# Optimization experiments

Measured on AMD Instinct MI355X. Metric: run time of the kernel, lower is better.

The kernel has to match this reference:

```python
import jax, jax.numpy as jnp
import numpy as np

B, C, D, H, W = 2, 64, 8, 24, 24  # hidden_dim = C; N = D*H*W = 4608 tokens


def setup_inputs() -> dict:
    key = jax.random.key(0)
    ks = jax.random.split(key, 8)
    s = 1.0 / np.sqrt(C)  # fan-in style init for 1x1 conv weights
    return {
        "x": jax.random.normal(ks[0], (B, C, D, H, W), dtype=jnp.float32),
        "h": jax.random.normal(ks[1], (B, C, D, H, W), dtype=jnp.float32),
        "Wq": jax.random.normal(ks[2], (C, C), dtype=jnp.float32) * s,
        "bq": jax.random.normal(ks[3], (C,), dtype=jnp.float32) * s,
        "Wk": jax.random.normal(ks[4], (C, C), dtype=jnp.float32) * s,
        "bk": jax.random.normal(ks[5], (C,), dtype=jnp.float32) * s,
        "Wv": jax.random.normal(ks[6], (C, C), dtype=jnp.float32) * s,
        "bv": jax.random.normal(ks[7], (C,), dtype=jnp.float32) * s,
    }


def reference(x, h, Wq, bq, Wk, bk, Wv, bv):
    # 1x1 Conv3d == per-token linear over channels
    def proj(inp, Wt, bt):
        f = inp.reshape(inp.shape[0], inp.shape[1], -1)  # [B, C, N]
        return jnp.einsum('oc,bcn->bon', Wt, f) + bt[None, :, None]

    q = proj(x, Wq, bq)  # [B, C, N]
    k = proj(h, Wk, bk)  # [B, C, N]
    v = proj(h, Wv, bv)  # [B, C, N]

    scale = 1.0 / np.sqrt(k.shape[1])  # k.size(1) ** 0.5 == sqrt(C)
    scores = jnp.einsum('bcm,bcn->bmn', q, k) * scale  # [B, N, N]
    attn = jax.nn.softmax(scores, axis=-1)
    out = jnp.einsum('bcn,bmn->bcm', v, attn)  # [B, C, N]
    return out.reshape(h.shape)
```

## Files before the change

### kernel.cpp

```cpp
#include <hip/hip_runtime.h>
#include <hip/hip_bf16.h>

#define C_DIM 64
#define N_TOK 4608
#define NBLK  72
#define B_SZ  2
#define M64BLKS 72
#define NSEG  8
#define SEGLEN (N_TOK / NSEG)
#define KTILES 288
#define VTILES 72
#define OSTR  68

typedef __bf16 bf16x8 __attribute__((ext_vector_type(8)));
typedef float  f32x4  __attribute__((ext_vector_type(4)));


__device__ __forceinline__ void gemm_tile(
    const __hip_bfloat16* wmat, const bf16x8 bin[2], const float* bias,
    int col, int quad, f32x4 acc[4])
{
    #pragma unroll
    for (int ot = 0; ot < 4; ot++) {
        f32x4 a = (f32x4){0.f, 0.f, 0.f, 0.f};
        #pragma unroll
        for (int kh = 0; kh < 2; kh++) {
            bf16x8 wf = *(const bf16x8*)(wmat + (ot * 16 + col) * 72 +
                                         kh * 32 + quad * 8);
            a = __builtin_amdgcn_mfma_f32_16x16x32_bf16(wf, bin[kh], a, 0, 0, 0);
        }
        float4 b4 = *(const float4*)(bias + ot * 16 + quad * 4);
        a[0] += b4.x; a[1] += b4.y; a[2] += b4.z; a[3] += b4.w;
        acc[ot] = a;
    }
}

__global__ __launch_bounds__(256) void proj_kernel(
    const float* __restrict__ x,  const float* __restrict__ h,
    const float* __restrict__ Wq, const float* __restrict__ bq,
    const float* __restrict__ Wk, const float* __restrict__ bk,
    const float* __restrict__ Wv, const float* __restrict__ bv,
    __hip_bfloat16* __restrict__ qS, __hip_bfloat16* __restrict__ kS,
    __hip_bfloat16* __restrict__ vS)
{
    __shared__ __hip_bfloat16 wl[3 * 64 * 72];
    __shared__ __hip_bfloat16 xt[64 * 72];
    __shared__ __hip_bfloat16 ht[64 * 72];
    __shared__ __hip_bfloat16 vl[64 * 72];

    const int b  = blockIdx.x / NBLK;
    const int n0 = (blockIdx.x % NBLK) * 64;
    const int t  = threadIdx.x;

    #pragma unroll
    for (int mat = 0; mat < 3; mat++) {
        const float* W = (mat == 0) ? Wq : ((mat == 1) ? Wk : Wv);
        __hip_bfloat16* wd = wl + mat * (64 * 72);
        #pragma unroll
        for (int i = 0; i < 4; i++) {
            const int ch = i * 256 + t;
            const int o = ch >> 4, c0 = (ch & 15) * 4;
            float4 w4 = *(const float4*)(W + ch * 4);
            union { __hip_bfloat16 e[4]; uint2 v; } pk;
            pk.e[0] = __float2bfloat16(w4.x); pk.e[1] = __float2bfloat16(w4.y);
            pk.e[2] = __float2bfloat16(w4.z); pk.e[3] = __float2bfloat16(w4.w);
            *(uint2*)(wd + o * 72 + c0) = pk.v;
        }
    }
    #pragma unroll
    for (int i = 0; i < 4; i++) {
        const int ch = i * 256 + t;
        const int c = ch >> 4, n4 = (ch & 15) * 4;
        float4 x4 = *(const float4*)(x + (size_t)(b * C_DIM + c) * N_TOK + n0 + n4);
        float4 h4 = *(const float4*)(h + (size_t)(b * C_DIM + c) * N_TOK + n0 + n4);
        xt[(n4 + 0) * 72 + c] = __float2bfloat16(x4.x);
        xt[(n4 + 1) * 72 + c] = __float2bfloat16(x4.y);
        xt[(n4 + 2) * 72 + c] = __float2bfloat16(x4.z);
        xt[(n4 + 3) * 72 + c] = __float2bfloat16(x4.w);
        ht[(n4 + 0) * 72 + c] = __float2bfloat16(h4.x);
        ht[(n4 + 1) * 72 + c] = __float2bfloat16(h4.y);
        ht[(n4 + 2) * 72 + c] = __float2bfloat16(h4.z);
        ht[(n4 + 3) * 72 + c] = __float2bfloat16(h4.w);
    }
    __syncthreads();

    const int wave = t >> 6, lane = t & 63;
    const int col = lane & 15, quad = lane >> 4;

    bf16x8 xb[2], hb[2];
    #pragma unroll
    for (int kh = 0; kh < 2; kh++) {
        xb[kh] = *(const bf16x8*)(xt + (wave * 16 + col) * 72 + kh * 32 + quad * 8);
        hb[kh] = *(const bf16x8*)(ht + (wave * 16 + col) * 72 + kh * 32 + quad * 8);
    }

    f32x4 acc[4];

    gemm_tile(wl + 0 * (64 * 72), xb, bq, col, quad, acc);
    {
        const size_t tile16 = (size_t)b * KTILES + (n0 >> 4) + wave;
        const float SC = 0.125f * 1.44269504088896f;
        #pragma unroll
        for (int ot = 0; ot < 4; ot++) {
            union { __hip_bfloat16 e[4]; uint2 v; } pk;
            #pragma unroll
            for (int r = 0; r < 4; r++) pk.e[r] = __float2bfloat16(acc[ot][r] * SC);
            *(uint2*)(qS + (tile16 << 10) + (ot >> 1) * 512 +
                      ((ot * 2 + (quad >> 1)) & 3) * 128 + col * 8 +
                      (quad & 1) * 4) = pk.v;
        }
    }

    gemm_tile(wl + 1 * (64 * 72), hb, bk, col, quad, acc);
    {
        const int t_l = (wave >> 1) * 2 + ((col >> 2) & 1);
        const int row = ((wave * 2 + (col >> 3)) & 3) * 4 + (col & 3);
        const size_t tile16 = (size_t)b * KTILES + (n0 >> 4) + t_l;
        #pragma unroll
        for (int ot = 0; ot < 4; ot++) {
            union { __hip_bfloat16 e[4]; uint2 v; } pk;
            #pragma unroll
            for (int r = 0; r < 4; r++) pk.e[r] = __float2bfloat16(acc[ot][r]);
            *(uint2*)(kS + (tile16 << 10) + (ot >> 1) * 512 +
                      ((ot * 2 + (quad >> 1)) & 3) * 128 + row * 8 +
                      (quad & 1) * 4) = pk.v;
        }
    }

    gemm_tile(wl + 2 * (64 * 72), hb, bv, col, quad, acc);
    #pragma unroll
    for (int ot = 0; ot < 4; ot++)
        #pragma unroll
        for (int r = 0; r < 4; r++)
            vl[(ot * 16 + quad * 4 + r) * 72 + wave * 16 + col] =
                __float2bfloat16(acc[ot][r]);
    __syncthreads();
    {
        const size_t vbase = ((size_t)(b * VTILES) + (n0 >> 6)) << 12;
        #pragma unroll
        for (int rep = 0; rep < 2; rep++) {
            const int ch = rep * 256 + t;
            const int cc = ch >> 7, hf = (ch >> 6) & 1;
            const int qd = (ch >> 4) & 3, c2 = ch & 15;
            *(uint4*)(vS + vbase + (size_t)ch * 8) =
                *(const uint4*)(vl + (cc * 16 + c2) * 72 + hf * 32 + qd * 8);
        }
    }
}

__global__ __launch_bounds__(512) void attn_kernel(
    const __hip_bfloat16* __restrict__ qS,
    const __hip_bfloat16* __restrict__ kS,
    const __hip_bfloat16* __restrict__ vS,
    float* __restrict__ out)
{
    __shared__ float o_lds[NSEG * 16 * OSTR];
    __shared__ float lstat[NSEG][64];

    const int b    = blockIdx.x / M64BLKS;
    const int mblk = blockIdx.x % M64BLKS;
    const int wave = threadIdx.x >> 6;
    const int lane = threadIdx.x & 63;
    const int col  = lane & 15;
    const int quad = lane >> 4;
    const int m0   = mblk * 64;

    const __hip_bfloat16* qp =
        qS + (((size_t)b * KTILES + (m0 >> 4)) << 10) + lane * 8;
    bf16x8 qa[4][2];
    #pragma unroll
    for (int ms = 0; ms < 4; ms++) {
        qa[ms][0] = *(const bf16x8*)(qp + ms * 1024);
        qa[ms][1] = *(const bf16x8*)(qp + ms * 1024 + 512);
    }

    f32x4 accO[4][4];
    #pragma unroll
    for (int ms = 0; ms < 4; ms++)
        #pragma unroll
        for (int cc = 0; cc < 4; cc++)
            accO[ms][cc] = (f32x4){0.f, 0.f, 0.f, 0.f};
    float rsum[4] = {0.f, 0.f, 0.f, 0.f};

    const int nbeg = wave * SEGLEN;

    #pragma unroll 1
    for (int n0 = nbeg; n0 < nbeg + SEGLEN; n0 += 64) {
        const __hip_bfloat16* kt =
            kS + (((size_t)b * KTILES + (n0 >> 4)) << 10) + lane * 8;
        bf16x8 ka[8];
        #pragma unroll
        for (int j = 0; j < 4; j++) {
            ka[2 * j]     = *(const bf16x8*)(kt + (j << 10));
            ka[2 * j + 1] = *(const bf16x8*)(kt + (j << 10) + 512);
        }
        const __hip_bfloat16* vt =
            vS + ((((size_t)b * VTILES) + (n0 >> 6)) << 12) + lane * 8;
        bf16x8 va[8];
        #pragma unroll
        for (int cc = 0; cc < 4; cc++) {
            va[2 * cc]     = *(const bf16x8*)(vt + cc * 1024);
            va[2 * cc + 1] = *(const bf16x8*)(vt + cc * 1024 + 512);
        }

        #pragma unroll
        for (int ms = 0; ms < 4; ms++) {
            f32x4 s[4];
            #pragma unroll
            for (int j = 0; j < 4; j++) {
                s[j] = __builtin_amdgcn_mfma_f32_16x16x32_bf16(
                           ka[2 * j], qa[ms][0], (f32x4){0.f, 0.f, 0.f, 0.f}, 0, 0, 0);
                s[j] = __builtin_amdgcn_mfma_f32_16x16x32_bf16(
                           ka[2 * j + 1], qa[ms][1], s[j], 0, 0, 0);
            }
            union { __hip_bfloat16 e[8]; bf16x8 v; } p0, p1;
            float ps = 0.f;
            #pragma unroll
            for (int j = 0; j < 2; j++)
                #pragma unroll
                for (int r = 0; r < 4; r++) {
                    float e0 = __builtin_amdgcn_exp2f(s[j][r]);
                    float e1 = __builtin_amdgcn_exp2f(s[2 + j][r]);
                    ps += e0 + e1;
                    p0.e[j * 4 + r] = __float2bfloat16(e0);
                    p1.e[j * 4 + r] = __float2bfloat16(e1);
                }
            rsum[ms] += ps;
            #pragma unroll
            for (int cc = 0; cc < 4; cc++) {
                accO[ms][cc] = __builtin_amdgcn_mfma_f32_16x16x32_bf16(
                                   va[2 * cc], p0.v, accO[ms][cc], 0, 0, 0);
                accO[ms][cc] = __builtin_amdgcn_mfma_f32_16x16x32_bf16(
                                   va[2 * cc + 1], p1.v, accO[ms][cc], 0, 0, 0);
            }
        }
    }

    #pragma unroll
    for (int ms = 0; ms < 4; ms++) {
        rsum[ms] += __shfl_xor(rsum[ms], 16);
        rsum[ms] += __shfl_xor(rsum[ms], 32);
    }
    if (quad == 0) {
        #pragma unroll
        for (int ms = 0; ms < 4; ms++) lstat[wave][ms * 16 + col] = rsum[ms];
    }

    #pragma unroll
    for (int phase = 0; phase < 4; phase++) {
        #pragma unroll
        for (int cc = 0; cc < 4; cc++)
            *(f32x4*)(o_lds + (wave * 16 + col) * OSTR + cc * 16 + quad * 4) =
                accO[phase][cc];
        __syncthreads();
        if (threadIdx.x < 256) {
            const int m  = threadIdx.x & 15;
            const int cq = threadIdx.x >> 4;
            const int mi = phase * 16 + m;
            float lsum = 0.f;
            f32x4 oacc = (f32x4){0.f, 0.f, 0.f, 0.f};
            #pragma unroll
            for (int sgm = 0; sgm < NSEG; sgm++) {
                lsum += lstat[sgm][mi];
                oacc += *(const f32x4*)(o_lds + (sgm * 16 + m) * OSTR + cq * 4);
            }
            const float inv = 1.0f / lsum;
            #pragma unroll
            for (int r = 0; r < 4; r++) {
                const int c = cq * 4 + r;
                out[(size_t)(b * C_DIM + c) * N_TOK + m0 + phase * 16 + m] =
                    oacc[r] * inv;
            }
        }
        __syncthreads();
    }
}

extern "C" void kernel_launch(void* const* d_in, const int* in_sizes, int n_in,
                              void* d_out, int out_size, void* d_ws, size_t ws_size,
                              hipStream_t stream) {
    const float* x  = (const float*)d_in[0];
    const float* h  = (const float*)d_in[1];
    const float* Wq = (const float*)d_in[2];
    const float* bq = (const float*)d_in[3];
    const float* Wk = (const float*)d_in[4];
    const float* bk = (const float*)d_in[5];
    const float* Wv = (const float*)d_in[6];
    const float* bv = (const float*)d_in[7];
    float* out = (float*)d_out;

    const size_t elems = (size_t)B_SZ * N_TOK * C_DIM;
    __hip_bfloat16* qS = (__hip_bfloat16*)d_ws;
    __hip_bfloat16* kS = qS + elems;
    __hip_bfloat16* vS = kS + elems;

    proj_kernel<<<B_SZ * NBLK, 256, 0, stream>>>(x, h, Wq, bq, Wk, bk, Wv, bv,
                                                 qS, kS, vS);
    attn_kernel<<<B_SZ * M64BLKS, 512, 0, stream>>>(qS, kS, vS, out);
}
```

Baseline: 93.16 us.

## Double-buffer K/V tiles into LDS via async global_load_lds with 32-token steps

Replaces the per-iteration direct global loads of K and V fragments into registers with asynchronous global-to-LDS copies into a per-wave double buffer, prefetching the next 32-token tile while computing the current one. The inner step shrinks from 64 to 32 tokens, which cuts the fragment registers needed and packs P into a single bf16x8 per m-subtile. The goal is to hide global memory latency and lower register pressure. In exchange it uses 128KB of LDS per block, which may limit occupancy to one block per CU, and adds a barrier before the reduction so the staging buffers can be reused as o_lds.

```diff
diff --git a/kernel.cpp b/kernel.cpp
--- a/kernel.cpp
+++ b/kernel.cpp
@@ -8,6 +8,7 @@
 #define M64BLKS 72
 #define NSEG  8
 #define SEGLEN (N_TOK / NSEG)
+#define NT32  (SEGLEN / 32)
 #define KTILES 288
 #define VTILES 72
 #define OSTR  68
@@ -15,6 +16,12 @@
 typedef __bf16 bf16x8 __attribute__((ext_vector_type(8)));
 typedef float  f32x4  __attribute__((ext_vector_type(4)));
 
+
+__device__ __forceinline__ void gll16(const void* g, void* l) {
+    __builtin_amdgcn_global_load_lds(
+        (const __attribute__((address_space(1))) void*)g,
+        (__attribute__((address_space(3))) void*)l, 16, 0, 0);
+}
 
 __device__ __forceinline__ void gemm_tile(
     const __hip_bfloat16* wmat, const bf16x8 bin[2], const float* bias,
@@ -154,8 +161,9 @@
     const __hip_bfloat16* __restrict__ vS,
     float* __restrict__ out)
 {
-    __shared__ float o_lds[NSEG * 16 * OSTR];
-    __shared__ float lstat[NSEG][64];
+    __shared__ __align__(16) char smem[NSEG * 16384];
+    float* o_lds = (float*)smem;
+    float* lstat = (float*)(smem + NSEG * 16 * OSTR * 4);
 
     const int b    = blockIdx.x / M64BLKS;
     const int mblk = blockIdx.x % M64BLKS;
@@ -183,56 +191,74 @@
     float rsum[4] = {0.f, 0.f, 0.f, 0.f};
 
     const int nbeg = wave * SEGLEN;
+    char* sbase = smem + wave * 16384;
+    const __hip_bfloat16* kbb = kS + (((size_t)b * KTILES) << 10) + lane * 8;
+    const __hip_bfloat16* vbb = vS + (((size_t)b * VTILES) << 12) + lane * 8;
+
+    auto stage = [&](int t, int p) {
+        const int n0 = nbeg + t * 32;
+        char* dst = sbase + p * 8192;
+        const __hip_bfloat16* kt = kbb + ((size_t)(n0 >> 4) << 10);
+        #pragma unroll
+        for (int j = 0; j < 2; j++) {
+            gll16(kt + (j << 10),       dst + j * 2048);
+            gll16(kt + (j << 10) + 512, dst + j * 2048 + 1024);
+        }
+        const __hip_bfloat16* vt = vbb + ((size_t)(n0 >> 6) << 12) +
+                                   ((n0 >> 5) & 1) * 512;
+        #pragma unroll
+        for (int cc = 0; cc < 4; cc++)
+            gll16(vt + cc * 1024, dst + 4096 + cc * 1024);
+    };
+
+    stage(0, 0);
 
     #pragma unroll 1
-    for (int n0 = nbeg; n0 < nbeg + SEGLEN; n0 += 64) {
-        const __hip_bfloat16* kt =
-            kS + (((size_t)b * KTILES + (n0 >> 4)) << 10) + lane * 8;
-        bf16x8 ka[8];
-        #pragma unroll
-        for (int j = 0; j < 4; j++) {
-            ka[2 * j]     = *(const bf16x8*)(kt + (j << 10));
-            ka[2 * j + 1] = *(const bf16x8*)(kt + (j << 10) + 512);
-        }
-        const __hip_bfloat16* vt =
-            vS + ((((size_t)b * VTILES) + (n0 >> 6)) << 12) + lane * 8;
-        bf16x8 va[8];
-        #pragma unroll
-        for (int cc = 0; cc < 4; cc++) {
-            va[2 * cc]     = *(const bf16x8*)(vt + cc * 1024);
-            va[2 * cc + 1] = *(const bf16x8*)(vt + cc * 1024 + 512);
-        }
+    for (int t = 0; t < NT32; t++) {
+        const int p = t & 1;
+        if (t + 1 < NT32) {
+            stage(t + 1, p ^ 1);
+            asm volatile("s_waitcnt vmcnt(8)" ::: "memory");
+        } else {
+            asm volatile("s_waitcnt vmcnt(0)" ::: "memory");
+        }
+        __builtin_amdgcn_sched_barrier(0);
+
+        const char* buf = sbase + p * 8192;
+        bf16x8 ka[4], va[4];
+        #pragma unroll
+        for (int j = 0; j < 2; j++) {
+            ka[2 * j]     = *(const bf16x8*)(buf + j * 2048 + lane * 16);
+            ka[2 * j + 1] = *(const bf16x8*)(buf + j * 2048 + 1024 + lane * 16);
+        }
+        #pragma unroll
+        for (int cc = 0; cc < 4; cc++)
+            va[cc] = *(const bf16x8*)(buf + 4096 + cc * 1024 + lane * 16);
 
         #pragma unroll
         for (int ms = 0; ms < 4; ms++) {
-            f32x4 s[4];
-            #pragma unroll
-            for (int j = 0; j < 4; j++) {
-                s[j] = __builtin_amdgcn_mfma_f32_16x16x32_bf16(
-                           ka[2 * j], qa[ms][0], (f32x4){0.f, 0.f, 0.f, 0.f}, 0, 0, 0);
-                s[j] = __builtin_amdgcn_mfma_f32_16x16x32_bf16(
-                           ka[2 * j + 1], qa[ms][1], s[j], 0, 0, 0);
+            f32x4 s0 = __builtin_amdgcn_mfma_f32_16x16x32_bf16(
+                           ka[0], qa[ms][0], (f32x4){0.f, 0.f, 0.f, 0.f}, 0, 0, 0);
+            s0 = __builtin_amdgcn_mfma_f32_16x16x32_bf16(ka[1], qa[ms][1], s0, 0, 0, 0);
+            f32x4 s1 = __builtin_amdgcn_mfma_f32_16x16x32_bf16(
+                           ka[2], qa[ms][0], (f32x4){0.f, 0.f, 0.f, 0.f}, 0, 0, 0);
+            s1 = __builtin_amdgcn_mfma_f32_16x16x32_bf16(ka[3], qa[ms][1], s1, 0, 0, 0);
+
+            union { __hip_bfloat16 e[8]; bf16x8 v; } pk;
+            float ps = 0.f;
+            #pragma unroll
+            for (int r = 0; r < 4; r++) {
+                float e0 = __builtin_amdgcn_exp2f(s0[r]);
+                float e1 = __builtin_amdgcn_exp2f(s1[r]);
+                ps += e0 + e1;
+                pk.e[r]     = __float2bfloat16(e0);
+                pk.e[4 + r] = __float2bfloat16(e1);
             }
-            union { __hip_bfloat16 e[8]; bf16x8 v; } p0, p1;
-            float ps = 0.f;
-            #pragma unroll
-            for (int j = 0; j < 2; j++)
-                #pragma unroll
-                for (int r = 0; r < 4; r++) {
-                    float e0 = __builtin_amdgcn_exp2f(s[j][r]);
-                    float e1 = __builtin_amdgcn_exp2f(s[2 + j][r]);
-                    ps += e0 + e1;
-                    p0.e[j * 4 + r] = __float2bfloat16(e0);
-                    p1.e[j * 4 + r] = __float2bfloat16(e1);
-                }
             rsum[ms] += ps;
             #pragma unroll
-            for (int cc = 0; cc < 4; cc++) {
+            for (int cc = 0; cc < 4; cc++)
                 accO[ms][cc] = __builtin_amdgcn_mfma_f32_16x16x32_bf16(
-                                   va[2 * cc], p0.v, accO[ms][cc], 0, 0, 0);
-                accO[ms][cc] = __builtin_amdgcn_mfma_f32_16x16x32_bf16(
-                                   va[2 * cc + 1], p1.v, accO[ms][cc], 0, 0, 0);
-            }
+                                   va[cc], pk.v, accO[ms][cc], 0, 0, 0);
         }
     }
 
@@ -241,9 +267,12 @@
         rsum[ms] += __shfl_xor(rsum[ms], 16);
         rsum[ms] += __shfl_xor(rsum[ms], 32);
     }
+
+    __syncthreads();
+
     if (quad == 0) {
         #pragma unroll
-        for (int ms = 0; ms < 4; ms++) lstat[wave][ms * 16 + col] = rsum[ms];
+        for (int ms = 0; ms < 4; ms++) lstat[wave * 64 + ms * 16 + col] = rsum[ms];
     }
 
     #pragma unroll
@@ -261,7 +290,7 @@
             f32x4 oacc = (f32x4){0.f, 0.f, 0.f, 0.f};
             #pragma unroll
             for (int sgm = 0; sgm < NSEG; sgm++) {
-                lsum += lstat[sgm][mi];
+                lsum += lstat[sgm * 64 + mi];
                 oacc += *(const f32x4*)(o_lds + (sgm * 16 + m) * OSTR + cq * 4);
             }
             const float inv = 1.0f / lsum;
```

Result: slower. 95.78 us (+2.8%).

## Split attention key range across blocks and add normalization reduction kernel

Applied to the files above, without the earlier changes.

Each attention block now covers 128 query rows, with two wave groups of 64, and one third of the key range, so the grid grows from 144 to 216 blocks. Partial unnormalized outputs and row sums go to workspace buffers. A new norm_kernel sums the three partials and divides by the row sum. This aims to fill more compute units and shorten the serial key loop per wave, at the cost of extra global traffic for the partials and one more kernel launch.

```diff
diff --git a/kernel.cpp b/kernel.cpp
--- a/kernel.cpp
+++ b/kernel.cpp
@@ -5,9 +5,11 @@
 #define N_TOK 4608
 #define NBLK  72
 #define B_SZ  2
-#define M64BLKS 72
-#define NSEG  8
-#define SEGLEN (N_TOK / NSEG)
+#define M128BLKS 36
+#define NSPLIT 3
+#define NSEG  4
+#define SEGLEN 384
+#define NT    6
 #define KTILES 288
 #define VTILES 72
 #define OSTR  68
@@ -152,18 +154,26 @@
     const __hip_bfloat16* __restrict__ qS,
     const __hip_bfloat16* __restrict__ kS,
     const __hip_bfloat16* __restrict__ vS,
-    float* __restrict__ out)
+    float* __restrict__ Pb, float* __restrict__ Lb)
 {
-    __shared__ float o_lds[NSEG * 16 * OSTR];
-    __shared__ float lstat[NSEG][64];
-
-    const int b    = blockIdx.x / M64BLKS;
-    const int mblk = blockIdx.x % M64BLKS;
+    __shared__ float o_lds[2][NSEG][16][OSTR];
+    __shared__ float lstat[2][NSEG][64];
+
+    const int idx  = blockIdx.x;
+    const int b    = idx / (M128BLKS * NSPLIT);
+    const int rem  = idx % (M128BLKS * NSPLIT);
+    const int mblk = rem / NSPLIT;
+    const int ns   = rem % NSPLIT;
     const int wave = threadIdx.x >> 6;
     const int lane = threadIdx.x & 63;
     const int col  = lane & 15;
     const int quad = lane >> 4;
-    const int m0   = mblk * 64;
+    const int mg   = wave >> 2;
+    const int seg  = wave & 3;
+    const int m0   = mblk * 128 + mg * 64;
+
+    float* Pns = Pb + (size_t)ns * (B_SZ * C_DIM * N_TOK);
+    float* Lns = Lb + (size_t)ns * (B_SZ * N_TOK);
 
     const __hip_bfloat16* qp =
         qS + (((size_t)b * KTILES + (m0 >> 4)) << 10) + lane * 8;
@@ -182,10 +192,11 @@
             accO[ms][cc] = (f32x4){0.f, 0.f, 0.f, 0.f};
     float rsum[4] = {0.f, 0.f, 0.f, 0.f};
 
-    const int nbeg = wave * SEGLEN;
+    const int nbeg = ns * (NSEG * SEGLEN) + seg * SEGLEN;
 
     #pragma unroll 1
-    for (int n0 = nbeg; n0 < nbeg + SEGLEN; n0 += 64) {
+    for (int t = 0; t < NT; t++) {
+        const int n0 = nbeg + t * 64;
         const __hip_bfloat16* kt =
             kS + (((size_t)b * KTILES + (n0 >> 4)) << 10) + lane * 8;
         bf16x8 ka[8];
@@ -209,7 +220,8 @@
             #pragma unroll
             for (int j = 0; j < 4; j++) {
                 s[j] = __builtin_amdgcn_mfma_f32_16x16x32_bf16(
-                           ka[2 * j], qa[ms][0], (f32x4){0.f, 0.f, 0.f, 0.f}, 0, 0, 0);
+                           ka[2 * j], qa[ms][0],
+                           (f32x4){0.f, 0.f, 0.f, 0.f}, 0, 0, 0);
                 s[j] = __builtin_amdgcn_mfma_f32_16x16x32_bf16(
                            ka[2 * j + 1], qa[ms][1], s[j], 0, 0, 0);
             }
@@ -243,37 +255,58 @@
     }
     if (quad == 0) {
         #pragma unroll
-        for (int ms = 0; ms < 4; ms++) lstat[wave][ms * 16 + col] = rsum[ms];
-    }
-
-    #pragma unroll
-    for (int phase = 0; phase < 4; phase++) {
+        for (int ms = 0; ms < 4; ms++) lstat[mg][seg][ms * 16 + col] = rsum[ms];
+    }
+
+    #pragma unroll
+    for (int p = 0; p < 4; p++) {
         #pragma unroll
         for (int cc = 0; cc < 4; cc++)
-            *(f32x4*)(o_lds + (wave * 16 + col) * OSTR + cc * 16 + quad * 4) =
-                accO[phase][cc];
+            *(f32x4*)(&o_lds[mg][seg][col][cc * 16 + quad * 4]) = accO[p][cc];
         __syncthreads();
-        if (threadIdx.x < 256) {
-            const int m  = threadIdx.x & 15;
-            const int cq = threadIdx.x >> 4;
-            const int mi = phase * 16 + m;
-            float lsum = 0.f;
-            f32x4 oacc = (f32x4){0.f, 0.f, 0.f, 0.f};
-            #pragma unroll
-            for (int sgm = 0; sgm < NSEG; sgm++) {
-                lsum += lstat[sgm][mi];
-                oacc += *(const f32x4*)(o_lds + (sgm * 16 + m) * OSTR + cq * 4);
-            }
-            const float inv = 1.0f / lsum;
-            #pragma unroll
-            for (int r = 0; r < 4; r++) {
-                const int c = cq * 4 + r;
-                out[(size_t)(b * C_DIM + c) * N_TOK + m0 + phase * 16 + m] =
-                    oacc[r] * inv;
-            }
+        {
+            const int t   = threadIdx.x;
+            const int mgR = t >> 8;
+            const int c   = (t >> 2) & 63;
+            const int mq  = t & 3;
+            f32x4 os = (f32x4){0.f, 0.f, 0.f, 0.f};
+            f32x4 ls = (f32x4){0.f, 0.f, 0.f, 0.f};
+            #pragma unroll
+            for (int sgm = 0; sgm < NSEG; sgm++)
+                #pragma unroll
+                for (int j = 0; j < 4; j++) {
+                    os[j] += o_lds[mgR][sgm][mq * 4 + j][c];
+                    ls[j] += lstat[mgR][sgm][p * 16 + mq * 4 + j];
+                }
+            const int mabs = mblk * 128 + mgR * 64 + p * 16 + mq * 4;
+            *(f32x4*)(Pns + ((size_t)b * C_DIM + c) * N_TOK + mabs) = os;
+            if (c == 0)
+                *(f32x4*)(Lns + (size_t)b * N_TOK + mabs) = ls;
         }
         __syncthreads();
     }
+}
+
+__global__ __launch_bounds__(256) void norm_kernel(
+    const float* __restrict__ Pb, const float* __restrict__ Lb,
+    float* __restrict__ out)
+{
+    const size_t stride = (size_t)B_SZ * C_DIM * N_TOK;
+    const size_t f = ((size_t)blockIdx.x * 256 + threadIdx.x) * 4;
+    f32x4 o = *(const f32x4*)(Pb + f) +
+              *(const f32x4*)(Pb + stride + f) +
+              *(const f32x4*)(Pb + 2 * stride + f);
+    const int b = (int)(f / ((size_t)C_DIM * N_TOK));
+    const int m = (int)(f % N_TOK);
+    const size_t lf = (size_t)b * N_TOK + m;
+    const size_t lstride = (size_t)B_SZ * N_TOK;
+    f32x4 l = *(const f32x4*)(Lb + lf) +
+              *(const f32x4*)(Lb + lstride + lf) +
+              *(const f32x4*)(Lb + 2 * lstride + lf);
+    f32x4 r;
+    #pragma unroll
+    for (int j = 0; j < 4; j++) r[j] = o[j] / l[j];
+    *(f32x4*)(out + f) = r;
 }
 
 extern "C" void kernel_launch(void* const* d_in, const int* in_sizes, int n_in,
@@ -293,8 +326,11 @@
     __hip_bfloat16* qS = (__hip_bfloat16*)d_ws;
     __hip_bfloat16* kS = qS + elems;
     __hip_bfloat16* vS = kS + elems;
+    float* Pb = (float*)(vS + elems);
+    float* Lb = Pb + NSPLIT * elems;
 
     proj_kernel<<<B_SZ * NBLK, 256, 0, stream>>>(x, h, Wq, bq, Wk, bk, Wv, bv,
                                                  qS, kS, vS);
-    attn_kernel<<<B_SZ * M64BLKS, 512, 0, stream>>>(qS, kS, vS, out);
-}
+    attn_kernel<<<B_SZ * M128BLKS * NSPLIT, 512, 0, stream>>>(qS, kS, vS, Pb, Lb);
+    norm_kernel<<<576, 256, 0, stream>>>(Pb, Lb, out);
+}
```

Result: no change. 92.31 us (median of 2 runs) (-0.9%).

## Fuse projection and attention into one cooperative kernel with grid sync

Applied to the files above, without the earlier changes.

Merges the projection and attention kernels into a single cooperative launch of 144 blocks of 512 threads. A grid-wide barrier separates writing Q/K/V to workspace from the attention phase. The projection is split so four waves compute Q while the other four compute K and V, and shared memory is aliased between the two phases. This removes the second kernel launch and the gap between kernels, at the cost of a grid sync and cooperative-launch overhead.

```diff
diff --git a/kernel.cpp b/kernel.cpp
--- a/kernel.cpp
+++ b/kernel.cpp
@@ -1,13 +1,14 @@
 #include <hip/hip_runtime.h>
+#include <hip/hip_cooperative_groups.h>
 #include <hip/hip_bf16.h>
 
 #define C_DIM 64
 #define N_TOK 4608
 #define NBLK  72
 #define B_SZ  2
-#define M64BLKS 72
 #define NSEG  8
 #define SEGLEN (N_TOK / NSEG)
+#define NT64  (SEGLEN / 64)
 #define KTILES 288
 #define VTILES 72
 #define OSTR  68
@@ -15,6 +16,8 @@
 typedef __bf16 bf16x8 __attribute__((ext_vector_type(8)));
 typedef float  f32x4  __attribute__((ext_vector_type(4)));
 
+
+namespace cg = cooperative_groups;
 
 __device__ __forceinline__ void gemm_tile(
     const __hip_bfloat16* wmat, const bf16x8 bin[2], const float* bias,
@@ -35,30 +38,34 @@
     }
 }
 
-__global__ __launch_bounds__(256) void proj_kernel(
+__global__ __launch_bounds__(512) void fused_kernel(
     const float* __restrict__ x,  const float* __restrict__ h,
     const float* __restrict__ Wq, const float* __restrict__ bq,
     const float* __restrict__ Wk, const float* __restrict__ bk,
     const float* __restrict__ Wv, const float* __restrict__ bv,
     __hip_bfloat16* __restrict__ qS, __hip_bfloat16* __restrict__ kS,
-    __hip_bfloat16* __restrict__ vS)
+    __hip_bfloat16* __restrict__ vS, float* __restrict__ out)
 {
-    __shared__ __hip_bfloat16 wl[3 * 64 * 72];
-    __shared__ __hip_bfloat16 xt[64 * 72];
-    __shared__ __hip_bfloat16 ht[64 * 72];
-    __shared__ __hip_bfloat16 vl[64 * 72];
-
-    const int b  = blockIdx.x / NBLK;
-    const int n0 = (blockIdx.x % NBLK) * 64;
-    const int t  = threadIdx.x;
+    __shared__ __align__(16) char smraw[55296];
+    __hip_bfloat16* wl = (__hip_bfloat16*)smraw;
+    __hip_bfloat16* xt = (__hip_bfloat16*)(smraw + 27648);
+    __hip_bfloat16* ht = (__hip_bfloat16*)(smraw + 36864);
+    __hip_bfloat16* vl = (__hip_bfloat16*)(smraw + 46080);
+    float* o_lds = (float*)smraw;
+    float* lstat = (float*)(smraw + 34816);
+
+    const int b   = blockIdx.x / NBLK;
+    const int nb  = blockIdx.x % NBLK;
+    const int t   = threadIdx.x;
+    const int n0b = nb * 64;
 
     #pragma unroll
     for (int mat = 0; mat < 3; mat++) {
         const float* W = (mat == 0) ? Wq : ((mat == 1) ? Wk : Wv);
         __hip_bfloat16* wd = wl + mat * (64 * 72);
         #pragma unroll
-        for (int i = 0; i < 4; i++) {
-            const int ch = i * 256 + t;
+        for (int i = 0; i < 2; i++) {
+            const int ch = i * 512 + t;
             const int o = ch >> 4, c0 = (ch & 15) * 4;
             float4 w4 = *(const float4*)(W + ch * 4);
             union { __hip_bfloat16 e[4]; uint2 v; } pk;
@@ -68,11 +75,11 @@
         }
     }
     #pragma unroll
-    for (int i = 0; i < 4; i++) {
-        const int ch = i * 256 + t;
+    for (int i = 0; i < 2; i++) {
+        const int ch = i * 512 + t;
         const int c = ch >> 4, n4 = (ch & 15) * 4;
-        float4 x4 = *(const float4*)(x + (size_t)(b * C_DIM + c) * N_TOK + n0 + n4);
-        float4 h4 = *(const float4*)(h + (size_t)(b * C_DIM + c) * N_TOK + n0 + n4);
+        float4 x4 = *(const float4*)(x + (size_t)(b * C_DIM + c) * N_TOK + n0b + n4);
+        float4 h4 = *(const float4*)(h + (size_t)(b * C_DIM + c) * N_TOK + n0b + n4);
         xt[(n4 + 0) * 72 + c] = __float2bfloat16(x4.x);
         xt[(n4 + 1) * 72 + c] = __float2bfloat16(x4.y);
         xt[(n4 + 2) * 72 + c] = __float2bfloat16(x4.z);
@@ -87,18 +94,15 @@
     const int wave = t >> 6, lane = t & 63;
     const int col = lane & 15, quad = lane >> 4;
 
-    bf16x8 xb[2], hb[2];
-    #pragma unroll
-    for (int kh = 0; kh < 2; kh++) {
-        xb[kh] = *(const bf16x8*)(xt + (wave * 16 + col) * 72 + kh * 32 + quad * 8);
-        hb[kh] = *(const bf16x8*)(ht + (wave * 16 + col) * 72 + kh * 32 + quad * 8);
-    }
-
-    f32x4 acc[4];
-
-    gemm_tile(wl + 0 * (64 * 72), xb, bq, col, quad, acc);
-    {
-        const size_t tile16 = (size_t)b * KTILES + (n0 >> 4) + wave;
+    if (wave < 4) {
+        bf16x8 xb[2];
+        #pragma unroll
+        for (int kh = 0; kh < 2; kh++)
+            xb[kh] = *(const bf16x8*)(xt + (wave * 16 + col) * 72 +
+                                      kh * 32 + quad * 8);
+        f32x4 acc[4];
+        gemm_tile(wl, xb, bq, col, quad, acc);
+        const size_t tile16 = (size_t)b * KTILES + (n0b >> 4) + wave;
         const float SC = 0.125f * 1.44269504088896f;
         #pragma unroll
         for (int ot = 0; ot < 4; ot++) {
@@ -109,61 +113,50 @@
                       ((ot * 2 + (quad >> 1)) & 3) * 128 + col * 8 +
                       (quad & 1) * 4) = pk.v;
         }
-    }
-
-    gemm_tile(wl + 1 * (64 * 72), hb, bk, col, quad, acc);
-    {
-        const int t_l = (wave >> 1) * 2 + ((col >> 2) & 1);
-        const int row = ((wave * 2 + (col >> 3)) & 3) * 4 + (col & 3);
-        const size_t tile16 = (size_t)b * KTILES + (n0 >> 4) + t_l;
-        #pragma unroll
-        for (int ot = 0; ot < 4; ot++) {
-            union { __hip_bfloat16 e[4]; uint2 v; } pk;
-            #pragma unroll
-            for (int r = 0; r < 4; r++) pk.e[r] = __float2bfloat16(acc[ot][r]);
-            *(uint2*)(kS + (tile16 << 10) + (ot >> 1) * 512 +
-                      ((ot * 2 + (quad >> 1)) & 3) * 128 + row * 8 +
-                      (quad & 1) * 4) = pk.v;
-        }
-    }
-
-    gemm_tile(wl + 2 * (64 * 72), hb, bv, col, quad, acc);
-    #pragma unroll
-    for (int ot = 0; ot < 4; ot++)
-        #pragma unroll
-        for (int r = 0; r < 4; r++)
-            vl[(ot * 16 + quad * 4 + r) * 72 + wave * 16 + col] =
-                __float2bfloat16(acc[ot][r]);
+    } else {
+        const int wv = wave - 4;
+        bf16x8 hb[2];
+        #pragma unroll
+        for (int kh = 0; kh < 2; kh++)
+            hb[kh] = *(const bf16x8*)(ht + (wv * 16 + col) * 72 +
+                                      kh * 32 + quad * 8);
+        f32x4 acc[4];
+        gemm_tile(wl + 1 * (64 * 72), hb, bk, col, quad, acc);
+        {
+            const int t_l = (wv >> 1) * 2 + ((col >> 2) & 1);
+            const int row = ((wv * 2 + (col >> 3)) & 3) * 4 + (col & 3);
+            const size_t tile16 = (size_t)b * KTILES + (n0b >> 4) + t_l;
+            #pragma unroll
+            for (int ot = 0; ot < 4; ot++) {
+                union { __hip_bfloat16 e[4]; uint2 v; } pk;
+                #pragma unroll
+                for (int r = 0; r < 4; r++) pk.e[r] = __float2bfloat16(acc[ot][r]);
+                *(uint2*)(kS + (tile16 << 10) + (ot >> 1) * 512 +
+                          ((ot * 2 + (quad >> 1)) & 3) * 128 + row * 8 +
+                          (quad & 1) * 4) = pk.v;
+            }
+        }
+        gemm_tile(wl + 2 * (64 * 72), hb, bv, col, quad, acc);
+        #pragma unroll
+        for (int ot = 0; ot < 4; ot++)
+            #pragma unroll
+            for (int r = 0; r < 4; r++)
+                vl[(ot * 16 + quad * 4 + r) * 72 + wv * 16 + col] =
+                    __float2bfloat16(acc[ot][r]);
+    }
     __syncthreads();
     {
-        const size_t vbase = ((size_t)(b * VTILES) + (n0 >> 6)) << 12;
-        #pragma unroll
-        for (int rep = 0; rep < 2; rep++) {
-            const int ch = rep * 256 + t;
-            const int cc = ch >> 7, hf = (ch >> 6) & 1;
-            const int qd = (ch >> 4) & 3, c2 = ch & 15;
-            *(uint4*)(vS + vbase + (size_t)ch * 8) =
-                *(const uint4*)(vl + (cc * 16 + c2) * 72 + hf * 32 + qd * 8);
-        }
-    }
-}
-
-__global__ __launch_bounds__(512) void attn_kernel(
-    const __hip_bfloat16* __restrict__ qS,
-    const __hip_bfloat16* __restrict__ kS,
-    const __hip_bfloat16* __restrict__ vS,
-    float* __restrict__ out)
-{
-    __shared__ float o_lds[NSEG * 16 * OSTR];
-    __shared__ float lstat[NSEG][64];
-
-    const int b    = blockIdx.x / M64BLKS;
-    const int mblk = blockIdx.x % M64BLKS;
-    const int wave = threadIdx.x >> 6;
-    const int lane = threadIdx.x & 63;
-    const int col  = lane & 15;
-    const int quad = lane >> 4;
-    const int m0   = mblk * 64;
+        const size_t vbase = ((size_t)(b * VTILES) + (n0b >> 6)) << 12;
+        const int cc = t >> 7, hf = (t >> 6) & 1;
+        const int qd = (t >> 4) & 3, c2 = t & 15;
+        *(uint4*)(vS + vbase + (size_t)t * 8) =
+            *(const uint4*)(vl + (cc * 16 + c2) * 72 + hf * 32 + qd * 8);
+    }
+
+    __threadfence();
+    cg::this_grid().sync();
+
+    const int m0 = nb * 64;
 
     const __hip_bfloat16* qp =
         qS + (((size_t)b * KTILES + (m0 >> 4)) << 10) + lane * 8;
@@ -185,7 +178,8 @@
     const int nbeg = wave * SEGLEN;
 
     #pragma unroll 1
-    for (int n0 = nbeg; n0 < nbeg + SEGLEN; n0 += 64) {
+    for (int tt = 0; tt < NT64; tt++) {
+        const int n0 = nbeg + tt * 64;
         const __hip_bfloat16* kt =
             kS + (((size_t)b * KTILES + (n0 >> 4)) << 10) + lane * 8;
         bf16x8 ka[8];
@@ -209,7 +203,8 @@
             #pragma unroll
             for (int j = 0; j < 4; j++) {
                 s[j] = __builtin_amdgcn_mfma_f32_16x16x32_bf16(
-                           ka[2 * j], qa[ms][0], (f32x4){0.f, 0.f, 0.f, 0.f}, 0, 0, 0);
+                           ka[2 * j], qa[ms][0],
+                           (f32x4){0.f, 0.f, 0.f, 0.f}, 0, 0, 0);
                 s[j] = __builtin_amdgcn_mfma_f32_16x16x32_bf16(
                            ka[2 * j + 1], qa[ms][1], s[j], 0, 0, 0);
             }
@@ -241,9 +236,10 @@
         rsum[ms] += __shfl_xor(rsum[ms], 16);
         rsum[ms] += __shfl_xor(rsum[ms], 32);
     }
+    __syncthreads();
     if (quad == 0) {
         #pragma unroll
-        for (int ms = 0; ms < 4; ms++) lstat[wave][ms * 16 + col] = rsum[ms];
+        for (int ms = 0; ms < 4; ms++) lstat[wave * 64 + ms * 16 + col] = rsum[ms];
     }
 
     #pragma unroll
@@ -261,7 +257,7 @@
             f32x4 oacc = (f32x4){0.f, 0.f, 0.f, 0.f};
             #pragma unroll
             for (int sgm = 0; sgm < NSEG; sgm++) {
-                lsum += lstat[sgm][mi];
+                lsum += lstat[sgm * 64 + mi];
                 oacc += *(const f32x4*)(o_lds + (sgm * 16 + m) * OSTR + cq * 4);
             }
             const float inv = 1.0f / lsum;
@@ -294,7 +290,9 @@
     __hip_bfloat16* kS = qS + elems;
     __hip_bfloat16* vS = kS + elems;
 
-    proj_kernel<<<B_SZ * NBLK, 256, 0, stream>>>(x, h, Wq, bq, Wk, bk, Wv, bv,
-                                                 qS, kS, vS);
-    attn_kernel<<<B_SZ * M64BLKS, 512, 0, stream>>>(qS, kS, vS, out);
+    void* args[] = { (void*)&x, (void*)&h, (void*)&Wq, (void*)&bq,
+                     (void*)&Wk, (void*)&bk, (void*)&Wv, (void*)&bv,
+                     (void*)&qS, (void*)&kS, (void*)&vS, (void*)&out };
+    hipLaunchCooperativeKernel((void*)fused_kernel,
+                               dim3(B_SZ * NBLK), dim3(512), args, 0, stream);
 }
```

Result: slower. 150.1 us (+61.2%).
